# Performance work log

Measured on AMD Instinct MI355X. Metric: run time of the kernel, lower is better.

Reference implementation:

```python
import jax, jax.numpy as jnp
import numpy as np

N_IN, N_H0, N_H1, N_H2, N_H3, N_OUT = 512, 1024, 1024, 1024, 512, 128
B, T = 128, 512
STD = 0.05


def setup_inputs() -> dict:
    key = jax.random.key(0)
    ks = jax.random.split(key, 7)
    # torch nn.Linear(in, out, bias=False) stores weight as [out, in]
    return {
        "input_spikes": jax.random.uniform(ks[0], (B, T, N_IN), dtype=jnp.float32),
        "W_in_h0": STD * jax.random.normal(ks[1], (N_H0, N_IN), dtype=jnp.float32),
        "W_h0_h1": STD * jax.random.normal(ks[2], (N_H1, N_H0), dtype=jnp.float32),
        "W_h1_h2": STD * jax.random.normal(ks[3], (N_H2, N_H1), dtype=jnp.float32),
        "W_h2_h2": STD * jax.random.normal(ks[4], (N_H2, N_H2), dtype=jnp.float32),
        "W_h2_h3": STD * jax.random.normal(ks[5], (N_H3, N_H2), dtype=jnp.float32),
        "W_h3_out": STD * jax.random.normal(ks[6], (N_OUT, N_H3), dtype=jnp.float32),
    }


def _lif(current, v, alpha, v_th):
    v = alpha * v + current
    s = (v >= v_th).astype(v.dtype)
    return s, v * (1.0 - s)


def reference(input_spikes, W_in_h0, W_h0_h1, W_h1_h2, W_h2_h2, W_h2_h3, W_h3_out):
    b = input_spikes.shape[0]
    dt = input_spikes.dtype
    z = lambda n: jnp.zeros((b, n), dtype=dt)
    # carry: membrane potentials for h0..h3, out, plus recurrent h2 spikes
    init = (z(N_H0), z(N_H1), z(N_H2), z(N_H3), z(N_OUT), z(N_H2))
    xs = jnp.swapaxes(input_spikes, 0, 1)  # [T, B, N_IN]

    def step(carry, x_t):
        v0, v1, v2, v3, vo, s2_prev = carry
        s0, v0 = _lif(x_t @ W_in_h0.T, v0, 0.9, 0.5)
        s1, v1 = _lif(s0 @ W_h0_h1.T, v1, 0.95, 0.5)
        s2, v2 = _lif(s1 @ W_h1_h2.T + s2_prev @ W_h2_h2.T, v2, 0.93, 0.5)
        s3, v3 = _lif(s2 @ W_h2_h3.T, v3, 0.9, 0.5)
        so, vo = _lif(s3 @ W_h3_out.T, vo, 0.82, 0.8)
        return (v0, v1, v2, v3, vo, s2), so

    _, out = jax.lax.scan(step, init, xs)
    output_spikes = jnp.swapaxes(out, 0, 1)  # [B, T, N_OUT]
    spike_counts = output_spikes.sum(axis=1)  # [B, N_OUT]
    return output_spikes, spike_counts
```

## Files before the change

kernel.cpp:

```cpp
#include <hip/hip_runtime.h>
#include <cstddef>


#define NB 128
#define NT 512

enum : size_t {
  OFF_V0   = 0,
  OFF_V1   = OFF_V0 + 131072,
  OFF_V2   = OFF_V1 + 131072,
  OFF_V3   = OFF_V2 + 131072,
  OFF_VO   = OFF_V3 + 65536,
  OFF_CNT  = OFF_VO + 16384,
  OFF_C2A  = OFF_CNT + 16384,
  OFF_BYTE = OFF_C2A + 262144,
  WS_FLOATS = OFF_BYTE + 229376
};
#define BS0 0
#define BS1 262144
#define BS2 524288
#define BS3 786432

__global__ __launch_bounds__(256) void init_kernel(float* __restrict__ wf) {
  size_t i = (size_t)blockIdx.x * blockDim.x + threadIdx.x;
  size_t stride = (size_t)gridDim.x * blockDim.x;
  for (size_t j = i; j < WS_FLOATS; j += stride) wf[j] = 0.0f;
}

__device__ __forceinline__ void wrA8(float (&A)[32][32], int ac, int ar, uint2 u) {
  A[ac + 0][ar] = (float)(u.x & 0xff);
  A[ac + 1][ar] = (float)((u.x >> 8) & 0xff);
  A[ac + 2][ar] = (float)((u.x >> 16) & 0xff);
  A[ac + 3][ar] = (float)(u.x >> 24);
  A[ac + 4][ar] = (float)(u.y & 0xff);
  A[ac + 5][ar] = (float)((u.y >> 8) & 0xff);
  A[ac + 6][ar] = (float)((u.y >> 16) & 0xff);
  A[ac + 7][ar] = (float)(u.y >> 24);
}
__device__ __forceinline__ void wrW16(float (&Wt)[32][68], int wk, int wr,
    const float4& w0, const float4& w1, const float4& w2, const float4& w3) {
  Wt[wk + 0][wr]      = w0.x; Wt[wk + 1][wr]      = w0.y;
  Wt[wk + 2][wr]      = w0.z; Wt[wk + 3][wr]      = w0.w;
  Wt[wk + 0][wr + 16] = w1.x; Wt[wk + 1][wr + 16] = w1.y;
  Wt[wk + 2][wr + 16] = w1.z; Wt[wk + 3][wr + 16] = w1.w;
  Wt[wk + 0][wr + 32] = w2.x; Wt[wk + 1][wr + 32] = w2.y;
  Wt[wk + 2][wr + 32] = w2.z; Wt[wk + 3][wr + 32] = w2.w;
  Wt[wk + 0][wr + 48] = w3.x; Wt[wk + 1][wr + 48] = w3.y;
  Wt[wk + 2][wr + 48] = w3.z; Wt[wk + 3][wr + 48] = w3.w;
}
__device__ __forceinline__ void wrA4f(float (&A)[32][32], int ac4, int ar, float4 f) {
  A[ac4 + 0][ar] = f.x; A[ac4 + 1][ar] = f.y;
  A[ac4 + 2][ar] = f.z; A[ac4 + 3][ar] = f.w;
}
__device__ __forceinline__ void wrA4b(float (&A)[32][32], int ac4, int ar, unsigned u) {
  A[ac4 + 0][ar] = (float)(u & 0xff);
  A[ac4 + 1][ar] = (float)((u >> 8) & 0xff);
  A[ac4 + 2][ar] = (float)((u >> 16) & 0xff);
  A[ac4 + 3][ar] = (float)(u >> 24);
}
__device__ __forceinline__ void wrW8(float (&Wt)[32][68], int wk2, int wr,
    const float4& w0, const float4& w1) {
  Wt[wk2 + 0][wr] = w0.x; Wt[wk2 + 1][wr] = w0.y;
  Wt[wk2 + 2][wr] = w0.z; Wt[wk2 + 3][wr] = w0.w;
  Wt[wk2 + 4][wr] = w1.x; Wt[wk2 + 5][wr] = w1.y;
  Wt[wk2 + 6][wr] = w1.z; Wt[wk2 + 7][wr] = w1.w;
}

__device__ __forceinline__ void gemm_split(
    const unsigned char* __restrict__ Abase, int Astride,
    const float* __restrict__ W,
    int bBase, int oBase,
    float (&As)[2][2][32][32], float (&Ws)[2][2][32][68],
    float (&pan)[4][4])
{
  const int tid = threadIdx.x;
  const int grp = tid >> 7, lt = tid & 127;
  const int ar = lt >> 2, ac = (lt & 3) << 3;
  const int wr = lt >> 3, wk = (lt & 7) << 2;
  const int tb4 = (lt >> 4) << 2;
  const int to4 = (lt & 15) << 2;
  const int kb = grp << 9;

  const unsigned char* Arow = Abase + (size_t)(bBase + ar) * Astride + kb + ac;
  const float* Wr = W + (size_t)(oBase + wr) * 1024 + kb + wk;

  {
    uint2 a = *(const uint2*)(Arow);
    float4 w0 = *(const float4*)(Wr);
    float4 w1 = *(const float4*)(Wr + 16 * 1024);
    float4 w2 = *(const float4*)(Wr + 32 * 1024);
    float4 w3 = *(const float4*)(Wr + 48 * 1024);
    wrA8(As[grp][0], ac, ar, a);
    wrW16(Ws[grp][0], wk, wr, w0, w1, w2, w3);
  }
  uint2 pa = *(const uint2*)(Arow + 32);
  float4 pw0 = *(const float4*)(Wr + 32);
  float4 pw1 = *(const float4*)(Wr + 32 + 16 * 1024);
  float4 pw2 = *(const float4*)(Wr + 32 + 32 * 1024);
  float4 pw3 = *(const float4*)(Wr + 32 + 48 * 1024);
  __syncthreads();

  int cb = 0;
#pragma unroll 1
  for (int kt = 0; kt < 16; ++kt) {
    uint2 na; float4 nw0, nw1, nw2, nw3;
    if (kt + 2 < 16) {
      const int ko = (kt + 2) << 5;
      na  = *(const uint2*)(Arow + ko);
      nw0 = *(const float4*)(Wr + ko);
      nw1 = *(const float4*)(Wr + ko + 16 * 1024);
      nw2 = *(const float4*)(Wr + ko + 32 * 1024);
      nw3 = *(const float4*)(Wr + ko + 48 * 1024);
    }
#pragma unroll
    for (int k = 0; k < 32; ++k) {
      const float4 a = *(const float4*)&As[grp][cb][k][tb4];
      const float4 w = *(const float4*)&Ws[grp][cb][k][to4];
      pan[0][0] = fmaf(a.x, w.x, pan[0][0]);
      pan[0][1] = fmaf(a.x, w.y, pan[0][1]);
      pan[0][2] = fmaf(a.x, w.z, pan[0][2]);
      pan[0][3] = fmaf(a.x, w.w, pan[0][3]);
      pan[1][0] = fmaf(a.y, w.x, pan[1][0]);
      pan[1][1] = fmaf(a.y, w.y, pan[1][1]);
      pan[1][2] = fmaf(a.y, w.z, pan[1][2]);
      pan[1][3] = fmaf(a.y, w.w, pan[1][3]);
      pan[2][0] = fmaf(a.z, w.x, pan[2][0]);
      pan[2][1] = fmaf(a.z, w.y, pan[2][1]);
      pan[2][2] = fmaf(a.z, w.z, pan[2][2]);
      pan[2][3] = fmaf(a.z, w.w, pan[2][3]);
      pan[3][0] = fmaf(a.w, w.x, pan[3][0]);
      pan[3][1] = fmaf(a.w, w.y, pan[3][1]);
      pan[3][2] = fmaf(a.w, w.z, pan[3][2]);
      pan[3][3] = fmaf(a.w, w.w, pan[3][3]);
    }
    if (kt + 1 < 16) {
      const int nb = cb ^ 1;
      wrA8(As[grp][nb], ac, ar, pa);
      wrW16(Ws[grp][nb], wk, wr, pw0, pw1, pw2, pw3);
    }
    if (kt + 2 < 16) { pa = na; pw0 = nw0; pw1 = nw1; pw2 = nw2; pw3 = nw3; }
    __syncthreads();
    cb ^= 1;
  }

  float* foldp = &As[1][0][0][0];
  if (grp == 1) {
#pragma unroll
    for (int i = 0; i < 4; ++i) {
      float4 st; st.x = pan[i][0]; st.y = pan[i][1];
      st.z = pan[i][2]; st.w = pan[i][3];
      *(float4*)&foldp[(i * 128 + lt) * 4] = st;
    }
  }
  __syncthreads();
  if (grp == 0) {
#pragma unroll
    for (int i = 0; i < 4; ++i) {
      float4 h = *(const float4*)&foldp[(i * 128 + lt) * 4];
      pan[i][0] = __fadd_rn(pan[i][0], h.x);
      pan[i][1] = __fadd_rn(pan[i][1], h.y);
      pan[i][2] = __fadd_rn(pan[i][2], h.z);
      pan[i][3] = __fadd_rn(pan[i][3], h.w);
    }
  }
}

template<bool AFLOAT>
__device__ __forceinline__ void gemm_whole(
    const void* __restrict__ Abase, int Astride,
    const float* __restrict__ W,
    int bBase, int oBase,
    float (&As)[2][2][32][32], float (&Ws)[2][2][32][68],
    float (&pan)[4][2])
{
  const int tid = threadIdx.x;
  const int ar = tid >> 3, ac4 = (tid & 7) << 2;
  const int wr = tid >> 2, wk2 = (tid & 3) << 3;
  const int tb4 = (tid >> 5) << 2;
  const int to2 = (tid & 31) << 1;

  const float* Af = (const float*)Abase + (size_t)(bBase + ar) * Astride + ac4;
  const unsigned char* Ab = (const unsigned char*)Abase + (size_t)(bBase + ar) * Astride + ac4;
  const float* Wr = W + (size_t)(oBase + wr) * 512 + wk2;

  {
    float4 w0 = *(const float4*)(Wr);
    float4 w1 = *(const float4*)(Wr + 4);
    if (AFLOAT) wrA4f(As[0][0], ac4, ar, *(const float4*)(Af));
    else        wrA4b(As[0][0], ac4, ar, *(const unsigned*)(Ab));
    wrW8(Ws[0][0], wk2, wr, w0, w1);
  }
  float4 paf; unsigned pab;
  if (AFLOAT) paf = *(const float4*)(Af + 32); else pab = *(const unsigned*)(Ab + 32);
  float4 pw0 = *(const float4*)(Wr + 32);
  float4 pw1 = *(const float4*)(Wr + 36);
  __syncthreads();

  int cb = 0;
#pragma unroll 1
  for (int kt = 0; kt < 16; ++kt) {
    float4 naf; unsigned nab; float4 nw0, nw1;
    if (kt + 2 < 16) {
      const int ko = (kt + 2) << 5;
      if (AFLOAT) naf = *(const float4*)(Af + ko); else nab = *(const unsigned*)(Ab + ko);
      nw0 = *(const float4*)(Wr + ko);
      nw1 = *(const float4*)(Wr + ko + 4);
    }
#pragma unroll
    for (int k = 0; k < 32; ++k) {
      const float4 a = *(const float4*)&As[0][cb][k][tb4];
      const float2 w = *(const float2*)&Ws[0][cb][k][to2];
      pan[0][0] = fmaf(a.x, w.x, pan[0][0]);
      pan[0][1] = fmaf(a.x, w.y, pan[0][1]);
      pan[1][0] = fmaf(a.y, w.x, pan[1][0]);
      pan[1][1] = fmaf(a.y, w.y, pan[1][1]);
      pan[2][0] = fmaf(a.z, w.x, pan[2][0]);
      pan[2][1] = fmaf(a.z, w.y, pan[2][1]);
      pan[3][0] = fmaf(a.w, w.x, pan[3][0]);
      pan[3][1] = fmaf(a.w, w.y, pan[3][1]);
    }
    if (kt + 1 < 16) {
      const int nb = cb ^ 1;
      if (AFLOAT) wrA4f(As[0][nb], ac4, ar, paf);
      else        wrA4b(As[0][nb], ac4, ar, pab);
      wrW8(Ws[0][nb], wk2, wr, pw0, pw1);
    }
    if (kt + 2 < 16) { paf = naf; pab = nab; pw0 = nw0; pw1 = nw1; }
    __syncthreads();
    cb ^= 1;
  }
}

__global__ __launch_bounds__(256) void phase_kernel(
    const float* __restrict__ x,
    const float* __restrict__ W0, const float* __restrict__ W1,
    const float* __restrict__ W2a, const float* __restrict__ W2b,
    const float* __restrict__ W3, const float* __restrict__ W4,
    float* __restrict__ wf, float* __restrict__ out, int p)
{
  __shared__ float As[2][2][32][32];
  __shared__ float Ws[2][2][32][68];

  float* cnt = wf + OFF_CNT;
  float* c2a = wf + OFF_C2A;
  unsigned char* sb = (unsigned char*)(wf + OFF_BYTE);
  const int cur = p & 1, prev = cur ^ 1;

  const int blk = blockIdx.x;
  int g, lb, t;
  if (blk < 64)       { g = 0; lb = blk;       t = p;     }
  else if (blk < 128) { g = 1; lb = blk - 64;  t = p - 1; }
  else if (blk < 192) { g = 2; lb = blk - 128; t = p - 2; }
  else if (blk < 256) { g = 3; lb = blk - 192; t = p - 3; }
  else if (blk < 288) { g = 4; lb = blk - 256; t = p - 4; }
  else                { g = 5; lb = blk - 288; t = p - 5; }
  if (t < 0 || t >= NT) return;

  const int ntO = (g == 4) ? 8 : (g == 5) ? 2 : 16;
  const int N   = (g == 4) ? 512 : (g == 5) ? 128 : 1024;
  const int bBase = (lb / ntO) << 5;
  const int oBase = (lb % ntO) << 6;
  const int tid = threadIdx.x;

  if (g == 0 || g == 5) {
    float pan[4][2] = {{0.f,0.f},{0.f,0.f},{0.f,0.f},{0.f,0.f}};
    float alpha, vth; float* v;
    if (g == 0) {
      gemm_whole<true >(x + (size_t)t * 512, NT * 512, W0, bBase, oBase, As, Ws, pan);
      alpha = 0.90f; vth = 0.5f; v = wf + OFF_V0;
    } else {
      gemm_whole<false>(sb + BS3 + (size_t)prev * 65536, 512, W4, bBase, oBase, As, Ws, pan);
      alpha = 0.82f; vth = 0.8f; v = wf + OFF_VO;
    }
    const int tb4 = (tid >> 5) << 2;
    const int to2 = (tid & 31) << 1;
    unsigned char* sOut = sb + BS0 + (size_t)cur * 131072;
#pragma unroll
    for (int i = 0; i < 4; ++i) {
      const int b = bBase + tb4 + i;
      int si[2];
#pragma unroll
      for (int j = 0; j < 2; ++j) {
        const int o = oBase + to2 + j;
        float* vp = v + (size_t)b * N + o;
        float vv = __fadd_rn(__fmul_rn(alpha, *vp), pan[i][j]);
        int s = (vv >= vth) ? 1 : 0;
        float sf = (float)s;
        *vp = __fmul_rn(vv, __fsub_rn(1.0f, sf));
        si[j] = s;
        if (g == 5) {
          out[(size_t)b * (NT * 128) + (size_t)t * 128 + o] = sf;
          cnt[b * 128 + o] = __fadd_rn(cnt[b * 128 + o], sf);
        }
      }
      if (g == 0) {
        *(unsigned short*)(sOut + (size_t)b * 1024 + oBase + to2) =
            (unsigned short)(si[0] | (si[1] << 8));
      }
    }
    return;
  }

  const unsigned char* Ab; const float* Wm;
  switch (g) {
    case 1: Ab = sb + BS0 + (size_t)prev * 131072; Wm = W1;  break;
    case 2: Ab = sb + BS1 + (size_t)prev * 131072; Wm = W2a; break;
    case 3: Ab = sb + BS2 + (size_t)prev * 131072; Wm = W2b; break;
    default: Ab = sb + BS2 + (size_t)prev * 131072; Wm = W3; break;
  }
  const int Astride = 1024;

  float pan[4][4];
#pragma unroll
  for (int i = 0; i < 4; ++i)
#pragma unroll
    for (int j = 0; j < 4; ++j) pan[i][j] = 0.f;

  gemm_split(Ab, Astride, Wm, bBase, oBase, As, Ws, pan);

  if (tid >= 128) return;
  const int lt = tid;
  const int tb4 = (lt >> 4) << 2;
  const int to4 = (lt & 15) << 2;

  if (g == 2) {
    float* dst = c2a + (size_t)cur * 131072;
#pragma unroll
    for (int i = 0; i < 4; ++i) {
      const int b = bBase + tb4 + i;
      float4 st; st.x = pan[i][0]; st.y = pan[i][1];
      st.z = pan[i][2]; st.w = pan[i][3];
      *(float4*)(dst + (size_t)b * 1024 + oBase + to4) = st;
    }
    return;
  }

  float alpha; float* v; unsigned char* sOut;
  switch (g) {
    case 1: alpha = 0.95f; v = wf + OFF_V1; sOut = sb + BS1 + (size_t)cur * 131072; break;
    case 3: alpha = 0.93f; v = wf + OFF_V2; sOut = sb + BS2 + (size_t)cur * 131072; break;
    default: alpha = 0.90f; v = wf + OFF_V3; sOut = sb + BS3 + (size_t)cur * 65536; break;
  }
  const float* c2aPrev = c2a + (size_t)prev * 131072;

#pragma unroll
  for (int i = 0; i < 4; ++i) {
    const int b = bBase + tb4 + i;
    float cin[4];
    if (g == 3) {
      float4 ca = *(const float4*)(c2aPrev + (size_t)b * 1024 + oBase + to4);
      cin[0] = __fadd_rn(ca.x, pan[i][0]);
      cin[1] = __fadd_rn(ca.y, pan[i][1]);
      cin[2] = __fadd_rn(ca.z, pan[i][2]);
      cin[3] = __fadd_rn(ca.w, pan[i][3]);
    } else {
      cin[0] = pan[i][0]; cin[1] = pan[i][1];
      cin[2] = pan[i][2]; cin[3] = pan[i][3];
    }
    unsigned packed = 0;
#pragma unroll
    for (int j = 0; j < 4; ++j) {
      const int o = oBase + to4 + j;
      float* vp = v + (size_t)b * N + o;
      float vv = __fadd_rn(__fmul_rn(alpha, *vp), cin[j]);
      int s = (vv >= 0.5f) ? 1 : 0;
      float sf = (float)s;
      *vp = __fmul_rn(vv, __fsub_rn(1.0f, sf));
      packed |= (unsigned)s << (8 * j);
    }
    *(unsigned*)(sOut + (size_t)b * N + oBase + to4) = packed;
  }
}

__global__ __launch_bounds__(256) void fin_kernel(const float* __restrict__ counts,
                                                  float* __restrict__ out) {
  int i = blockIdx.x * blockDim.x + threadIdx.x;
  if (i < 128 * 128) out[(size_t)128 * NT * 128 + i] = counts[i];
}

extern "C" void kernel_launch(void* const* d_in, const int* in_sizes, int n_in,
                              void* d_out, int out_size, void* d_ws, size_t ws_size,
                              hipStream_t stream) {
  const float* x   = (const float*)d_in[0];
  const float* W0  = (const float*)d_in[1];
  const float* W1  = (const float*)d_in[2];
  const float* W2a = (const float*)d_in[3];
  const float* W2b = (const float*)d_in[4];
  const float* W3  = (const float*)d_in[5];
  const float* W4  = (const float*)d_in[6];
  float* wf  = (float*)d_ws;
  float* out = (float*)d_out;

  init_kernel<<<512, 256, 0, stream>>>(wf);
  for (int p = 0; p < NT + 5; ++p) {
    phase_kernel<<<296, 256, 0, stream>>>(x, W0, W1, W2a, W2b, W3, W4, wf, out, p);
  }
  fin_kernel<<<64, 256, 0, stream>>>(wf + OFF_CNT, out);
}
```

Measured before the change: 24.41 ms.

## Replace per-step kernel launches with persistent cooperative kernel using grid sync

Replaces the 517 separate phase kernel launches plus the init and finalize kernels with a single cooperative persistent kernel of 296 blocks. Consecutive pipeline phases are separated by grid.sync() barriers instead of kernel boundaries, and zero-init and the count copy are folded in. This targets per-launch overhead and inter-kernel gaps; the cost is grid-wide barrier latency, and it needs all 296 blocks co-resident, with the old multi-launch path kept as a fallback if the cooperative launch fails.

```diff
diff --git a/kernel.cpp b/kernel.cpp
--- a/kernel.cpp
+++ b/kernel.cpp
@@ -1,5 +1,8 @@
 #include <hip/hip_runtime.h>
+#include <hip/hip_cooperative_groups.h>
 #include <cstddef>
+
+namespace cg = cooperative_groups;
 
 
 #define NB 128
@@ -20,12 +23,6 @@
 #define BS1 262144
 #define BS2 524288
 #define BS3 786432
-
-__global__ __launch_bounds__(256) void init_kernel(float* __restrict__ wf) {
-  size_t i = (size_t)blockIdx.x * blockDim.x + threadIdx.x;
-  size_t stride = (size_t)gridDim.x * blockDim.x;
-  for (size_t j = i; j < WS_FLOATS; j += stride) wf[j] = 0.0f;
-}
 
 __device__ __forceinline__ void wrA8(float (&A)[32][32], int ac, int ar, uint2 u) {
   A[ac + 0][ar] = (float)(u.x & 0xff);
@@ -231,30 +228,19 @@
   }
 }
 
-__global__ __launch_bounds__(256) void phase_kernel(
+__device__ __forceinline__ void do_phase(
+    int g, int lb, int t, int p,
     const float* __restrict__ x,
     const float* __restrict__ W0, const float* __restrict__ W1,
     const float* __restrict__ W2a, const float* __restrict__ W2b,
     const float* __restrict__ W3, const float* __restrict__ W4,
-    float* __restrict__ wf, float* __restrict__ out, int p)
+    float* __restrict__ wf, float* __restrict__ out,
+    float (&As)[2][2][32][32], float (&Ws)[2][2][32][68])
 {
-  __shared__ float As[2][2][32][32];
-  __shared__ float Ws[2][2][32][68];
-
   float* cnt = wf + OFF_CNT;
   float* c2a = wf + OFF_C2A;
   unsigned char* sb = (unsigned char*)(wf + OFF_BYTE);
   const int cur = p & 1, prev = cur ^ 1;
-
-  const int blk = blockIdx.x;
-  int g, lb, t;
-  if (blk < 64)       { g = 0; lb = blk;       t = p;     }
-  else if (blk < 128) { g = 1; lb = blk - 64;  t = p - 1; }
-  else if (blk < 192) { g = 2; lb = blk - 128; t = p - 2; }
-  else if (blk < 256) { g = 3; lb = blk - 192; t = p - 3; }
-  else if (blk < 288) { g = 4; lb = blk - 256; t = p - 4; }
-  else                { g = 5; lb = blk - 288; t = p - 5; }
-  if (t < 0 || t >= NT) return;
 
   const int ntO = (g == 4) ? 8 : (g == 5) ? 2 : 16;
   const int N   = (g == 4) ? 512 : (g == 5) ? 128 : 1024;
@@ -298,78 +284,150 @@
             (unsigned short)(si[0] | (si[1] << 8));
       }
     }
-    return;
-  }
-
-  const unsigned char* Ab; const float* Wm;
-  switch (g) {
-    case 1: Ab = sb + BS0 + (size_t)prev * 131072; Wm = W1;  break;
-    case 2: Ab = sb + BS1 + (size_t)prev * 131072; Wm = W2a; break;
-    case 3: Ab = sb + BS2 + (size_t)prev * 131072; Wm = W2b; break;
-    default: Ab = sb + BS2 + (size_t)prev * 131072; Wm = W3; break;
-  }
-  const int Astride = 1024;
-
-  float pan[4][4];
-#pragma unroll
-  for (int i = 0; i < 4; ++i)
-#pragma unroll
-    for (int j = 0; j < 4; ++j) pan[i][j] = 0.f;
-
-  gemm_split(Ab, Astride, Wm, bBase, oBase, As, Ws, pan);
-
-  if (tid >= 128) return;
-  const int lt = tid;
-  const int tb4 = (lt >> 4) << 2;
-  const int to4 = (lt & 15) << 2;
-
-  if (g == 2) {
-    float* dst = c2a + (size_t)cur * 131072;
-#pragma unroll
-    for (int i = 0; i < 4; ++i) {
-      const int b = bBase + tb4 + i;
-      float4 st; st.x = pan[i][0]; st.y = pan[i][1];
-      st.z = pan[i][2]; st.w = pan[i][3];
-      *(float4*)(dst + (size_t)b * 1024 + oBase + to4) = st;
-    }
-    return;
-  }
-
-  float alpha; float* v; unsigned char* sOut;
-  switch (g) {
-    case 1: alpha = 0.95f; v = wf + OFF_V1; sOut = sb + BS1 + (size_t)cur * 131072; break;
-    case 3: alpha = 0.93f; v = wf + OFF_V2; sOut = sb + BS2 + (size_t)cur * 131072; break;
-    default: alpha = 0.90f; v = wf + OFF_V3; sOut = sb + BS3 + (size_t)cur * 65536; break;
-  }
-  const float* c2aPrev = c2a + (size_t)prev * 131072;
-
-#pragma unroll
-  for (int i = 0; i < 4; ++i) {
-    const int b = bBase + tb4 + i;
-    float cin[4];
-    if (g == 3) {
-      float4 ca = *(const float4*)(c2aPrev + (size_t)b * 1024 + oBase + to4);
-      cin[0] = __fadd_rn(ca.x, pan[i][0]);
-      cin[1] = __fadd_rn(ca.y, pan[i][1]);
-      cin[2] = __fadd_rn(ca.z, pan[i][2]);
-      cin[3] = __fadd_rn(ca.w, pan[i][3]);
-    } else {
-      cin[0] = pan[i][0]; cin[1] = pan[i][1];
-      cin[2] = pan[i][2]; cin[3] = pan[i][3];
-    }
-    unsigned packed = 0;
-#pragma unroll
-    for (int j = 0; j < 4; ++j) {
-      const int o = oBase + to4 + j;
-      float* vp = v + (size_t)b * N + o;
-      float vv = __fadd_rn(__fmul_rn(alpha, *vp), cin[j]);
-      int s = (vv >= 0.5f) ? 1 : 0;
-      float sf = (float)s;
-      *vp = __fmul_rn(vv, __fsub_rn(1.0f, sf));
-      packed |= (unsigned)s << (8 * j);
-    }
-    *(unsigned*)(sOut + (size_t)b * N + oBase + to4) = packed;
-  }
+  } else {
+    const unsigned char* Ab; const float* Wm;
+    switch (g) {
+      case 1: Ab = sb + BS0 + (size_t)prev * 131072; Wm = W1;  break;
+      case 2: Ab = sb + BS1 + (size_t)prev * 131072; Wm = W2a; break;
+      case 3: Ab = sb + BS2 + (size_t)prev * 131072; Wm = W2b; break;
+      default: Ab = sb + BS2 + (size_t)prev * 131072; Wm = W3; break;
+    }
+
+    float pan[4][4];
+#pragma unroll
+    for (int i = 0; i < 4; ++i)
+#pragma unroll
+      for (int j = 0; j < 4; ++j) pan[i][j] = 0.f;
+
+    gemm_split(Ab, 1024, Wm, bBase, oBase, As, Ws, pan);
+
+    if (tid < 128) {
+      const int lt = tid;
+      const int tb4 = (lt >> 4) << 2;
+      const int to4 = (lt & 15) << 2;
+
+      if (g == 2) {
+        float* dst = c2a + (size_t)cur * 131072;
+#pragma unroll
+        for (int i = 0; i < 4; ++i) {
+          const int b = bBase + tb4 + i;
+          float4 st; st.x = pan[i][0]; st.y = pan[i][1];
+          st.z = pan[i][2]; st.w = pan[i][3];
+          *(float4*)(dst + (size_t)b * 1024 + oBase + to4) = st;
+        }
+      } else {
+        float alpha; float* v; unsigned char* sOut;
+        switch (g) {
+          case 1: alpha = 0.95f; v = wf + OFF_V1; sOut = sb + BS1 + (size_t)cur * 131072; break;
+          case 3: alpha = 0.93f; v = wf + OFF_V2; sOut = sb + BS2 + (size_t)cur * 131072; break;
+          default: alpha = 0.90f; v = wf + OFF_V3; sOut = sb + BS3 + (size_t)cur * 65536; break;
+        }
+        const float* c2aPrev = c2a + (size_t)prev * 131072;
+#pragma unroll
+        for (int i = 0; i < 4; ++i) {
+          const int b = bBase + tb4 + i;
+          float cin[4];
+          if (g == 3) {
+            float4 ca = *(const float4*)(c2aPrev + (size_t)b * 1024 + oBase + to4);
+            cin[0] = __fadd_rn(ca.x, pan[i][0]);
+            cin[1] = __fadd_rn(ca.y, pan[i][1]);
+            cin[2] = __fadd_rn(ca.z, pan[i][2]);
+            cin[3] = __fadd_rn(ca.w, pan[i][3]);
+          } else {
+            cin[0] = pan[i][0]; cin[1] = pan[i][1];
+            cin[2] = pan[i][2]; cin[3] = pan[i][3];
+          }
+          unsigned packed = 0;
+#pragma unroll
+          for (int j = 0; j < 4; ++j) {
+            const int o = oBase + to4 + j;
+            float* vp = v + (size_t)b * N + o;
+            float vv = __fadd_rn(__fmul_rn(alpha, *vp), cin[j]);
+            int s = (vv >= 0.5f) ? 1 : 0;
+            float sf = (float)s;
+            *vp = __fmul_rn(vv, __fsub_rn(1.0f, sf));
+            packed |= (unsigned)s << (8 * j);
+          }
+          *(unsigned*)(sOut + (size_t)b * N + oBase + to4) = packed;
+        }
+      }
+    }
+  }
+}
+
+__global__ __launch_bounds__(256, 2) void persist_kernel(
+    const float* __restrict__ x,
+    const float* __restrict__ W0, const float* __restrict__ W1,
+    const float* __restrict__ W2a, const float* __restrict__ W2b,
+    const float* __restrict__ W3, const float* __restrict__ W4,
+    float* __restrict__ wf, float* __restrict__ out)
+{
+  cg::grid_group grid = cg::this_grid();
+  __shared__ float As[2][2][32][32];
+  __shared__ float Ws[2][2][32][68];
+
+  {
+    size_t i = (size_t)blockIdx.x * blockDim.x + threadIdx.x;
+    size_t stride = (size_t)gridDim.x * blockDim.x;
+    for (size_t j = i; j < WS_FLOATS; j += stride) wf[j] = 0.0f;
+  }
+  grid.sync();
+
+  const int blk = blockIdx.x;
+  int g, lb, dt;
+  if (blk < 64)       { g = 0; lb = blk;       dt = 0; }
+  else if (blk < 128) { g = 1; lb = blk - 64;  dt = 1; }
+  else if (blk < 192) { g = 2; lb = blk - 128; dt = 2; }
+  else if (blk < 256) { g = 3; lb = blk - 192; dt = 3; }
+  else if (blk < 288) { g = 4; lb = blk - 256; dt = 4; }
+  else                { g = 5; lb = blk - 288; dt = 5; }
+
+  for (int p = 0; p < NT + 5; ++p) {
+    const int t = p - dt;
+    if (t >= 0 && t < NT) {
+      do_phase(g, lb, t, p, x, W0, W1, W2a, W2b, W3, W4, wf, out, As, Ws);
+    }
+    __syncthreads();
+    grid.sync();
+  }
+
+  {
+    size_t i = (size_t)blockIdx.x * blockDim.x + threadIdx.x;
+    size_t stride = (size_t)gridDim.x * blockDim.x;
+    for (size_t j = i; j < 16384; j += stride)
+      out[(size_t)128 * NT * 128 + j] = wf[OFF_CNT + j];
+  }
+}
+
+
+__global__ __launch_bounds__(256) void init_kernel(float* __restrict__ wf) {
+  size_t i = (size_t)blockIdx.x * blockDim.x + threadIdx.x;
+  size_t stride = (size_t)gridDim.x * blockDim.x;
+  for (size_t j = i; j < WS_FLOATS; j += stride) wf[j] = 0.0f;
+}
+
+__global__ __launch_bounds__(256) void phase_kernel(
+    const float* __restrict__ x,
+    const float* __restrict__ W0, const float* __restrict__ W1,
+    const float* __restrict__ W2a, const float* __restrict__ W2b,
+    const float* __restrict__ W3, const float* __restrict__ W4,
+    float* __restrict__ wf, float* __restrict__ out, int p)
+{
+  __shared__ float As[2][2][32][32];
+  __shared__ float Ws[2][2][32][68];
+
+  const int blk = blockIdx.x;
+  int g, lb, dt;
+  if (blk < 64)       { g = 0; lb = blk;       dt = 0; }
+  else if (blk < 128) { g = 1; lb = blk - 64;  dt = 1; }
+  else if (blk < 192) { g = 2; lb = blk - 128; dt = 2; }
+  else if (blk < 256) { g = 3; lb = blk - 192; dt = 3; }
+  else if (blk < 288) { g = 4; lb = blk - 256; dt = 4; }
+  else                { g = 5; lb = blk - 288; dt = 5; }
+  const int t = p - dt;
+  if (t < 0 || t >= NT) return;
+
+  do_phase(g, lb, t, p, x, W0, W1, W2a, W2b, W3, W4, wf, out, As, Ws);
 }
 
 __global__ __launch_bounds__(256) void fin_kernel(const float* __restrict__ counts,
@@ -377,6 +435,7 @@
   int i = blockIdx.x * blockDim.x + threadIdx.x;
   if (i < 128 * 128) out[(size_t)128 * NT * 128 + i] = counts[i];
 }
+
 
 extern "C" void kernel_launch(void* const* d_in, const int* in_sizes, int n_in,
                               void* d_out, int out_size, void* d_ws, size_t ws_size,
@@ -391,9 +450,26 @@
   float* wf  = (float*)d_ws;
   float* out = (float*)d_out;
 
-  init_kernel<<<512, 256, 0, stream>>>(wf);
-  for (int p = 0; p < NT + 5; ++p) {
-    phase_kernel<<<296, 256, 0, stream>>>(x, W0, W1, W2a, W2b, W3, W4, wf, out, p);
-  }
-  fin_kernel<<<64, 256, 0, stream>>>(wf + OFF_CNT, out);
-}
+  void* args[9];
+  args[0] = (void*)&x;
+  args[1] = (void*)&W0;
+  args[2] = (void*)&W1;
+  args[3] = (void*)&W2a;
+  args[4] = (void*)&W2b;
+  args[5] = (void*)&W3;
+  args[6] = (void*)&W4;
+  args[7] = (void*)&wf;
+  args[8] = (void*)&out;
+
+  hipError_t e = hipLaunchCooperativeKernel(
+      (const void*)persist_kernel, dim3(296), dim3(256), args, 0, stream);
+
+  if (e != hipSuccess) {
+    (void)hipGetLastError();
+    init_kernel<<<512, 256, 0, stream>>>(wf);
+    for (int p = 0; p < NT + 5; ++p) {
+      phase_kernel<<<296, 256, 0, stream>>>(x, W0, W1, W2a, W2b, W3, W4, wf, out, p);
+    }
+    fin_kernel<<<64, 256, 0, stream>>>(wf + OFF_CNT, out);
+  }
+}
```

After: 77.43 ms. 3.17x slower.
